# Performance work log

Measured on AMD Instinct MI355X. Metric: run time of the kernel, lower is better.

## Reference

```python
import jax, jax.numpy as jnp
import numpy as np
from jax.ops import segment_sum

N_NODES = 100000
IN, HID, OUT = 512, 128, 40
N_EDGES = 1600000


def gcn_conv(x, W, b, src, dst, n):
    # x: [N, d_in] -> linear transform first (PyG GCNConv applies lin before propagate)
    h = x @ W  # [N, d_out]
    # add self-loops
    loop = jnp.arange(n, dtype=src.dtype)
    s = jnp.concatenate([src, loop])
    d = jnp.concatenate([dst, loop])
    # symmetric normalization deg^{-1/2}[s] * deg^{-1/2}[d], deg over targets incl. self-loops
    deg = segment_sum(jnp.ones_like(d, dtype=h.dtype), d, num_segments=n)
    dinv = jnp.where(deg > 0, jax.lax.rsqrt(deg), 0.0)
    norm = dinv[s] * dinv[d]  # [E+N]
    msg = h[s] * norm[:, None]  # gather + scale
    out = segment_sum(msg, d, num_segments=n)  # scatter-add over edges
    return out + b


def setup_inputs() -> dict:
    key = jax.random.key(0)
    k1, k2, k3, k4, k5, k6 = jax.random.split(key, 6)
    x = jax.random.normal(k1, (N_NODES, IN), dtype=jnp.float32)
    edge_index = jax.random.randint(k2, (2, N_EDGES), 0, N_NODES, dtype=jnp.int64)
    s1 = 1.0 / np.sqrt(IN)
    s2 = 1.0 / np.sqrt(HID)
    W1 = jax.random.uniform(k3, (IN, HID), jnp.float32, -s1, s1)
    b1 = jnp.zeros((HID,), jnp.float32)
    W2 = jax.random.uniform(k4, (HID, OUT), jnp.float32, -s2, s2)
    b2 = jnp.zeros((OUT,), jnp.float32)
    return {"x": x, "edge_index": edge_index, "W1": W1, "b1": b1, "W2": W2, "b2": b2}


def reference(x, edge_index, W1, b1, W2, b2):
    src, dst = edge_index[0], edge_index[1]
    n = x.shape[0]
    # CRD: GCNConv -> relu (dropout is identity in eval mode)
    h = jax.nn.relu(gcn_conv(x, W1, b1, src, dst, n))
    # CLS: GCNConv -> log_softmax
    out = gcn_conv(h, W2, b2, src, dst, n)
    return jax.nn.log_softmax(out, axis=1)
```

## Files before the change

### kernel.cpp

```cpp
#include <hip/hip_runtime.h>
#include <hip/hip_bf16.h>

typedef unsigned short u16;
typedef __attribute__((ext_vector_type(8))) short short8;
typedef __attribute__((ext_vector_type(4))) float f32x4;

#define NN   100000
#define NE   1600000
#define DIN  512
#define DHID 128
#define DOUT 40
#define NB   98

__device__ __forceinline__ float bf2f(u16 u) {
  union { unsigned int i; float f; } v; v.i = ((unsigned int)u) << 16; return v.f;
}
__device__ __forceinline__ u16 f2bf(float f) {
  __hip_bfloat16 h = __float2bfloat16(f);
  return *reinterpret_cast<u16*>(&h);
}


__global__ __launch_bounds__(256) void k_count(const int* __restrict__ ei, int* __restrict__ cnt) {
  int e = blockIdx.x * 256 + threadIdx.x;
  int d = ei[NE + e];
  atomicAdd(&cnt[d], 1);
}

__global__ __launch_bounds__(256) void k_dinv(const int* __restrict__ cnt, float* __restrict__ dinv) {
  int i = blockIdx.x * 256 + threadIdx.x;
  if (i < NN) dinv[i] = rsqrtf((float)(cnt[i] + 1));
}

__global__ __launch_bounds__(256) void k_blocksum(const int* __restrict__ cnt, int* __restrict__ bsum) {
  __shared__ int s[256];
  int b = blockIdx.x, t = threadIdx.x;
  int base = b * 1024 + t * 4;
  int tot = 0;
  if (base < NN) { int4 v = *(const int4*)&cnt[base]; tot = v.x + v.y + v.z + v.w; }
  s[t] = tot; __syncthreads();
  for (int o = 128; o > 0; o >>= 1) { if (t < o) s[t] += s[t + o]; __syncthreads(); }
  if (t == 0) bsum[b] = s[0];
}

__global__ __launch_bounds__(128) void k_scanbsum(int* __restrict__ bsum) {
  __shared__ int s[128];
  int t = threadIdx.x;
  int v = (t < NB) ? bsum[t] : 0;
  s[t] = v; __syncthreads();
  for (int o = 1; o < 128; o <<= 1) {
    int add = (t >= o) ? s[t - o] : 0;
    __syncthreads();
    s[t] += add;
    __syncthreads();
  }
  if (t < NB) bsum[t] = s[t] - v;
}

__global__ __launch_bounds__(256) void k_scan3(const int* __restrict__ cnt, const int* __restrict__ bsum,
                                               int* __restrict__ offs) {
  __shared__ int s[256];
  int b = blockIdx.x, t = threadIdx.x;
  int base = b * 1024 + t * 4;
  int4 v = make_int4(0, 0, 0, 0);
  if (base < NN) v = *(const int4*)&cnt[base];
  int tot = v.x + v.y + v.z + v.w;
  s[t] = tot; __syncthreads();
  for (int o = 1; o < 256; o <<= 1) {
    int add = (t >= o) ? s[t - o] : 0;
    __syncthreads();
    s[t] += add;
    __syncthreads();
  }
  int tp = s[t] - tot;
  int b0 = bsum[b] + tp;
  if (base < NN) {
    int4 o4;
    o4.x = b0;
    o4.y = b0 + v.x;
    o4.z = b0 + v.x + v.y;
    o4.w = b0 + v.x + v.y + v.z;
    *(int4*)&offs[base] = o4;
  }
  if (b == 0 && t == 0) offs[NN] = NE;
}

__global__ __launch_bounds__(256) void k_scatter(const int* __restrict__ ei, const int* __restrict__ offs,
                                                 int* __restrict__ cursor, int* __restrict__ csr) {
  int e = blockIdx.x * 256 + threadIdx.x;
  int srcv = ei[e];
  int d = ei[NE + e];
  int pos = offs[d] + atomicAdd(&cursor[d], 1);
  csr[pos] = srcv;
}


__global__ __launch_bounds__(256) void k_prepw(const float* __restrict__ W1, u16* __restrict__ wt) {
  int id = blockIdx.x * 256 + threadIdx.x;
  int k = id & 511, n = id >> 9;
  wt[n * DIN + k] = f2bf(W1[k * DHID + n]);
}


__global__ __launch_bounds__(256) void k_gemm1(const float* __restrict__ x, const u16* __restrict__ wt,
                                               u16* __restrict__ h1) {
  __shared__ u16 xs[64][72];
  __shared__ u16 ws[128][72];
  int t = threadIdx.x;
  int row0 = blockIdx.x * 64;
  int w = t >> 6, l = t & 63;
  int lm = l & 15, lq = l >> 4;
  int mbase = w * 16;
  f32x4 acc[8];
#pragma unroll
  for (int nt = 0; nt < 8; nt++) acc[nt] = (f32x4){0.f, 0.f, 0.f, 0.f};

  for (int c = 0; c < 8; c++) {
    int k0 = c * 64;
#pragma unroll
    for (int it = 0; it < 4; it++) {
      int u = t + it * 256;
      int row = u >> 4, seg = u & 15;
      int gr = row0 + row;
      float4 v = make_float4(0.f, 0.f, 0.f, 0.f);
      if (gr < NN) v = *(const float4*)&x[gr * DIN + k0 + seg * 4];
      ushort4 o;
      o.x = f2bf(v.x); o.y = f2bf(v.y); o.z = f2bf(v.z); o.w = f2bf(v.w);
      *(ushort4*)&xs[row][seg * 4] = o;
    }
#pragma unroll
    for (int it = 0; it < 4; it++) {
      int u = t + it * 256;
      int n = u >> 3, seg = u & 7;
      *(uint4*)&ws[n][seg * 8] = *(const uint4*)&wt[n * DIN + k0 + seg * 8];
    }
    __syncthreads();
#pragma unroll
    for (int s = 0; s < 2; s++) {
      short8 a = *(const short8*)&xs[mbase + lm][s * 32 + lq * 8];
#pragma unroll
      for (int nt = 0; nt < 8; nt++) {
        short8 b = *(const short8*)&ws[nt * 16 + lm][s * 32 + lq * 8];
        acc[nt] = __builtin_amdgcn_mfma_f32_16x16x32_bf16(a, b, acc[nt], 0, 0, 0);
      }
    }
    __syncthreads();
  }
#pragma unroll
  for (int reg = 0; reg < 4; reg++) {
    int gr = row0 + mbase + lq * 4 + reg;
    if (gr < NN) {
#pragma unroll
      for (int nt = 0; nt < 8; nt++) {
        h1[gr * DHID + nt * 16 + lm] = f2bf(acc[nt][reg]);
      }
    }
  }
}


__global__ __launch_bounds__(128) void k_prop1(const u16* __restrict__ h1, const float* __restrict__ dinv,
                                               const int* __restrict__ offs, const int* __restrict__ csr,
                                               const float* __restrict__ b1, u16* __restrict__ g) {
  int n = blockIdx.x, f = threadIdx.x;
  float dn = dinv[n];
  float acc = b1[f] + dn * dn * bf2f(h1[n * DHID + f]);
  int p = offs[n], p1 = offs[n + 1];
  for (; p + 4 <= p1; p += 4) {
    int s0 = csr[p], s1 = csr[p + 1], s2 = csr[p + 2], s3 = csr[p + 3];
    float w0 = dinv[s0], w1 = dinv[s1], w2 = dinv[s2], w3 = dinv[s3];
    float v0 = bf2f(h1[s0 * DHID + f]);
    float v1 = bf2f(h1[s1 * DHID + f]);
    float v2 = bf2f(h1[s2 * DHID + f]);
    float v3 = bf2f(h1[s3 * DHID + f]);
    acc += dn * (w0 * v0 + w1 * v1 + w2 * v2 + w3 * v3);
  }
  for (; p < p1; p++) {
    int s0 = csr[p];
    acc += dn * dinv[s0] * bf2f(h1[s0 * DHID + f]);
  }
  g[n * DHID + f] = f2bf(fmaxf(acc, 0.f));
}


__global__ __launch_bounds__(320) void k_gemm2(const u16* __restrict__ g, const float* __restrict__ W2,
                                               u16* __restrict__ h2) {
  __shared__ float w2s[DHID][DOUT];
  __shared__ float gs[8][DHID];
  int t = threadIdx.x;
  int row0 = blockIdx.x * 8;
  for (int idx = t; idx < DHID * DOUT; idx += 320) ((float*)w2s)[idx] = W2[idx];
  for (int idx = t; idx < 8 * DHID; idx += 320) {
    int r = idx >> 7, k = idx & 127;
    int gr = row0 + r;
    ((float*)gs)[idx] = (gr < NN) ? bf2f(g[gr * DHID + k]) : 0.f;
  }
  __syncthreads();
  int r = t / DOUT, c = t % DOUT;
  float acc = 0.f;
#pragma unroll
  for (int k = 0; k < DHID; k += 4) {
    float4 gv = *(const float4*)&gs[r][k];
    acc += gv.x * w2s[k][c] + gv.y * w2s[k + 1][c] + gv.z * w2s[k + 2][c] + gv.w * w2s[k + 3][c];
  }
  int gr = row0 + r;
  if (gr < NN) h2[gr * DOUT + c] = f2bf(acc);
}


__global__ __launch_bounds__(64) void k_prop2(const u16* __restrict__ h2, const float* __restrict__ dinv,
                                              const int* __restrict__ offs, const int* __restrict__ csr,
                                              const float* __restrict__ b2, float* __restrict__ out) {
  int n = blockIdx.x, c = threadIdx.x;
  bool act = c < DOUT;
  float dn = dinv[n];
  float acc = act ? (b2[c] + dn * dn * bf2f(h2[n * DOUT + c])) : 0.f;
  int p = offs[n], p1 = offs[n + 1];
  for (; p + 4 <= p1; p += 4) {
    int s0 = csr[p], s1 = csr[p + 1], s2 = csr[p + 2], s3 = csr[p + 3];
    float w0 = dinv[s0], w1 = dinv[s1], w2 = dinv[s2], w3 = dinv[s3];
    float v0 = act ? bf2f(h2[s0 * DOUT + c]) : 0.f;
    float v1 = act ? bf2f(h2[s1 * DOUT + c]) : 0.f;
    float v2 = act ? bf2f(h2[s2 * DOUT + c]) : 0.f;
    float v3 = act ? bf2f(h2[s3 * DOUT + c]) : 0.f;
    acc += dn * (w0 * v0 + w1 * v1 + w2 * v2 + w3 * v3);
  }
  for (; p < p1; p++) {
    int s0 = csr[p];
    float v0 = act ? bf2f(h2[s0 * DOUT + c]) : 0.f;
    acc += dn * dinv[s0] * v0;
  }
  float logit = act ? acc : -INFINITY;
  float mx = logit;
#pragma unroll
  for (int o = 32; o > 0; o >>= 1) mx = fmaxf(mx, __shfl_xor(mx, o));
  float pv = act ? __expf(logit - mx) : 0.f;
  float sm = pv;
#pragma unroll
  for (int o = 32; o > 0; o >>= 1) sm += __shfl_xor(sm, o);
  if (act) out[n * DOUT + c] = logit - mx - logf(sm);
}


extern "C" void kernel_launch(void* const* d_in, const int* in_sizes, int n_in,
                              void* d_out, int out_size, void* d_ws, size_t ws_size,
                              hipStream_t stream) {
  const float* x  = (const float*)d_in[0];
  const int* ei   = (const int*)d_in[1];
  const float* W1 = (const float*)d_in[2];
  const float* b1 = (const float*)d_in[3];
  const float* W2 = (const float*)d_in[4];
  const float* b2 = (const float*)d_in[5];
  float* out      = (float*)d_out;

  char* ws = (char*)d_ws;
  int*   cnt    = (int*)(ws + 0);
  int*   cursor = (int*)(ws + 400000);
  float* dinv   = (float*)(ws + 800000);
  int*   offs   = (int*)(ws + 1200000);
  int*   bsum   = (int*)(ws + 1600128);
  int*   csr    = (int*)(ws + 1600640);
  u16*   h1     = (u16*)(ws + 8000640);
  u16*   g      = (u16*)(ws + 33600640);
  u16*   h2     = (u16*)(ws + 8000640);
  u16*   wt     = (u16*)(ws + 59200640);

  hipMemsetAsync(ws, 0, 800000, stream);

  k_count   <<<NE / 256, 256, 0, stream>>>(ei, cnt);
  k_dinv    <<<(NN + 255) / 256, 256, 0, stream>>>(cnt, dinv);
  k_blocksum<<<NB, 256, 0, stream>>>(cnt, bsum);
  k_scanbsum<<<1, 128, 0, stream>>>(bsum);
  k_scan3   <<<NB, 256, 0, stream>>>(cnt, bsum, offs);
  k_scatter <<<NE / 256, 256, 0, stream>>>(ei, offs, cursor, csr);

  k_prepw   <<<(DIN * DHID) / 256, 256, 0, stream>>>(W1, wt);
  k_gemm1   <<<(NN + 63) / 64, 256, 0, stream>>>(x, wt, h1);
  k_prop1   <<<NN, 128, 0, stream>>>(h1, dinv, offs, csr, b1, g);
  k_gemm2   <<<(NN + 7) / 8, 320, 0, stream>>>(g, W2, h2);
  k_prop2   <<<NN, 64, 0, stream>>>(h2, dinv, offs, csr, b2, out);
}
```

Measured before the change: 752.8 us.

## Precompute per-edge source weights in CSR and vectorize layer-1 propagation

The scatter kernel now stores dinv[src] alongside each CSR entry, so both propagation kernels read a contiguous weight array instead of doing a dependent random gather into dinv. Layer-1 propagation moves from a 128-thread block with scalar bf16 loads to a single 64-lane wavefront. Each lane loads four features as ushort4, the two half-waves process alternating edges, and a shuffle combines them. Common factors of dn are also hoisted out of the inner loops. The cost is an extra 6.4 MB written during CSR build and re-read during propagation.

```diff
diff --git a/kernel.cpp b/kernel.cpp
--- a/kernel.cpp
+++ b/kernel.cpp
@@ -86,12 +86,14 @@
 }
 
 __global__ __launch_bounds__(256) void k_scatter(const int* __restrict__ ei, const int* __restrict__ offs,
-                                                 int* __restrict__ cursor, int* __restrict__ csr) {
+                                                 int* __restrict__ cursor, const float* __restrict__ dinv,
+                                                 int* __restrict__ csr, float* __restrict__ wgt) {
   int e = blockIdx.x * 256 + threadIdx.x;
   int srcv = ei[e];
   int d = ei[NE + e];
   int pos = offs[d] + atomicAdd(&cursor[d], 1);
   csr[pos] = srcv;
+  wgt[pos] = dinv[srcv];
 }
 
 
@@ -159,27 +161,50 @@
 }
 
 
-__global__ __launch_bounds__(128) void k_prop1(const u16* __restrict__ h1, const float* __restrict__ dinv,
-                                               const int* __restrict__ offs, const int* __restrict__ csr,
-                                               const float* __restrict__ b1, u16* __restrict__ g) {
-  int n = blockIdx.x, f = threadIdx.x;
+__global__ __launch_bounds__(64) void k_prop1(const u16* __restrict__ h1, const float* __restrict__ dinv,
+                                              const int* __restrict__ offs, const int* __restrict__ csr,
+                                              const float* __restrict__ wgt, const float* __restrict__ b1,
+                                              u16* __restrict__ g) {
+  int n = blockIdx.x;
+  int l = threadIdx.x;
+  int half = l >> 5, c = l & 31;
+  int fb = c * 4;
   float dn = dinv[n];
-  float acc = b1[f] + dn * dn * bf2f(h1[n * DHID + f]);
-  int p = offs[n], p1 = offs[n + 1];
-  for (; p + 4 <= p1; p += 4) {
-    int s0 = csr[p], s1 = csr[p + 1], s2 = csr[p + 2], s3 = csr[p + 3];
-    float w0 = dinv[s0], w1 = dinv[s1], w2 = dinv[s2], w3 = dinv[s3];
-    float v0 = bf2f(h1[s0 * DHID + f]);
-    float v1 = bf2f(h1[s1 * DHID + f]);
-    float v2 = bf2f(h1[s2 * DHID + f]);
-    float v3 = bf2f(h1[s3 * DHID + f]);
-    acc += dn * (w0 * v0 + w1 * v1 + w2 * v2 + w3 * v3);
-  }
-  for (; p < p1; p++) {
-    int s0 = csr[p];
-    acc += dn * dinv[s0] * bf2f(h1[s0 * DHID + f]);
-  }
-  g[n * DHID + f] = f2bf(fmaxf(acc, 0.f));
+  float ax = 0.f, ay = 0.f, az = 0.f, aw = 0.f;
+  if (half == 0) {
+    ushort4 sv = *(const ushort4*)&h1[n * DHID + fb];
+    ax = dn * bf2f(sv.x); ay = dn * bf2f(sv.y); az = dn * bf2f(sv.z); aw = dn * bf2f(sv.w);
+  }
+  int p1e = offs[n + 1];
+  int q = offs[n] + half;
+  for (; q + 2 < p1e; q += 4) {
+    int s0 = csr[q], s1 = csr[q + 2];
+    float w0 = wgt[q], w1 = wgt[q + 2];
+    ushort4 v0 = *(const ushort4*)&h1[s0 * DHID + fb];
+    ushort4 v1 = *(const ushort4*)&h1[s1 * DHID + fb];
+    ax += w0 * bf2f(v0.x) + w1 * bf2f(v1.x);
+    ay += w0 * bf2f(v0.y) + w1 * bf2f(v1.y);
+    az += w0 * bf2f(v0.z) + w1 * bf2f(v1.z);
+    aw += w0 * bf2f(v0.w) + w1 * bf2f(v1.w);
+  }
+  if (q < p1e) {
+    int s0 = csr[q];
+    float w0 = wgt[q];
+    ushort4 v0 = *(const ushort4*)&h1[s0 * DHID + fb];
+    ax += w0 * bf2f(v0.x); ay += w0 * bf2f(v0.y);
+    az += w0 * bf2f(v0.z); aw += w0 * bf2f(v0.w);
+  }
+  ax += __shfl_xor(ax, 32); ay += __shfl_xor(ay, 32);
+  az += __shfl_xor(az, 32); aw += __shfl_xor(aw, 32);
+  if (half == 0) {
+    float4 bv = *(const float4*)&b1[fb];
+    ushort4 o;
+    o.x = f2bf(fmaxf(bv.x + dn * ax, 0.f));
+    o.y = f2bf(fmaxf(bv.y + dn * ay, 0.f));
+    o.z = f2bf(fmaxf(bv.z + dn * az, 0.f));
+    o.w = f2bf(fmaxf(bv.w + dn * aw, 0.f));
+    *(ushort4*)&g[n * DHID + fb] = o;
+  }
 }
 
 
@@ -210,27 +235,29 @@
 
 __global__ __launch_bounds__(64) void k_prop2(const u16* __restrict__ h2, const float* __restrict__ dinv,
                                               const int* __restrict__ offs, const int* __restrict__ csr,
-                                              const float* __restrict__ b2, float* __restrict__ out) {
+                                              const float* __restrict__ wgt, const float* __restrict__ b2,
+                                              float* __restrict__ out) {
   int n = blockIdx.x, c = threadIdx.x;
   bool act = c < DOUT;
   float dn = dinv[n];
-  float acc = act ? (b2[c] + dn * dn * bf2f(h2[n * DOUT + c])) : 0.f;
+  float accE = 0.f;
+  float self = act ? (dn * bf2f(h2[n * DOUT + c])) : 0.f;
   int p = offs[n], p1 = offs[n + 1];
   for (; p + 4 <= p1; p += 4) {
     int s0 = csr[p], s1 = csr[p + 1], s2 = csr[p + 2], s3 = csr[p + 3];
-    float w0 = dinv[s0], w1 = dinv[s1], w2 = dinv[s2], w3 = dinv[s3];
+    float w0 = wgt[p], w1 = wgt[p + 1], w2 = wgt[p + 2], w3 = wgt[p + 3];
     float v0 = act ? bf2f(h2[s0 * DOUT + c]) : 0.f;
     float v1 = act ? bf2f(h2[s1 * DOUT + c]) : 0.f;
     float v2 = act ? bf2f(h2[s2 * DOUT + c]) : 0.f;
     float v3 = act ? bf2f(h2[s3 * DOUT + c]) : 0.f;
-    acc += dn * (w0 * v0 + w1 * v1 + w2 * v2 + w3 * v3);
+    accE += w0 * v0 + w1 * v1 + w2 * v2 + w3 * v3;
   }
   for (; p < p1; p++) {
     int s0 = csr[p];
     float v0 = act ? bf2f(h2[s0 * DOUT + c]) : 0.f;
-    acc += dn * dinv[s0] * v0;
-  }
-  float logit = act ? acc : -INFINITY;
+    accE += wgt[p] * v0;
+  }
+  float logit = act ? (b2[c] + dn * (self + accE)) : -INFINITY;
   float mx = logit;
 #pragma unroll
   for (int o = 32; o > 0; o >>= 1) mx = fmaxf(mx, __shfl_xor(mx, o));
@@ -264,6 +291,7 @@
   u16*   g      = (u16*)(ws + 33600640);
   u16*   h2     = (u16*)(ws + 8000640);
   u16*   wt     = (u16*)(ws + 59200640);
+  float* wgt    = (float*)(ws + 59331712);
 
   hipMemsetAsync(ws, 0, 800000, stream);
 
@@ -272,11 +300,11 @@
   k_blocksum<<<NB, 256, 0, stream>>>(cnt, bsum);
   k_scanbsum<<<1, 128, 0, stream>>>(bsum);
   k_scan3   <<<NB, 256, 0, stream>>>(cnt, bsum, offs);
-  k_scatter <<<NE / 256, 256, 0, stream>>>(ei, offs, cursor, csr);
+  k_scatter <<<NE / 256, 256, 0, stream>>>(ei, offs, cursor, dinv, csr, wgt);
 
   k_prepw   <<<(DIN * DHID) / 256, 256, 0, stream>>>(W1, wt);
   k_gemm1   <<<(NN + 63) / 64, 256, 0, stream>>>(x, wt, h1);
-  k_prop1   <<<NN, 128, 0, stream>>>(h1, dinv, offs, csr, b1, g);
+  k_prop1   <<<NN, 64, 0, stream>>>(h1, dinv, offs, csr, wgt, b1, g);
   k_gemm2   <<<(NN + 7) / 8, 320, 0, stream>>>(g, W2, h2);
-  k_prop2   <<<NN, 64, 0, stream>>>(h2, dinv, offs, csr, b2, out);
-}
+  k_prop2   <<<NN, 64, 0, stream>>>(h2, dinv, offs, csr, wgt, b2, out);
+}
```

New measurement: 757.7 us. About the same (+0.6%).
